# Performance work log

Hardware: AMD Instinct MI355X
Metric: run time of the kernel (lower is better)

## Reference

```python
import jax, jax.numpy as jnp
import numpy as np

DIM = 768
HEADS = 12
DHEAD = 64
N = 197  # 1 cls token + 14*14 patches
P = 196
KMAX = 9  # max neighborhood size (interior patch: 3x3 window)
SCALE = DHEAD ** -0.5


def _build_neighbors():
    """Reproduce the module's hard-coded kv_list; pad to KMAX with a mask."""
    top = set(range(2, 14))
    down = set(range(184, 196))
    left = set(range(15, 170, 14))
    right = set(range(28, 183, 14))
    idx = np.zeros((P, KMAX), np.int32)
    msk = np.zeros((P, KMAX), np.float32)
    for i in range(1, 197):
        if i == 1:
            nb = [1, 2, 15, 16]
        elif i == 14:
            nb = [13, 14, 27, 28]
        elif i == 183:
            nb = [169, 170, 183, 184]
        elif i == 196:
            nb = [181, 182, 195, 196]
        elif i in top:
            nb = [i - 1, i, i + 1, i + 13, i + 14, i + 15]
        elif i in left:
            nb = [i - 14, i - 13, i, i + 1, i + 14, i + 15]
        elif i in right:
            nb = [i - 15, i - 14, i - 1, i, i + 13, i + 14]
        elif i in down:
            nb = [i - 15, i - 14, i - 13, i - 1, i, i + 1]
        else:
            nb = [i - 15, i - 14, i - 13, i - 1, i, i + 1, i + 13, i + 14, i + 15]
        L = len(nb)
        idx[i - 1, :L] = nb
        msk[i - 1, :L] = 1.0
    return jnp.asarray(idx), jnp.asarray(msk)

NBR_IDX, NBR_MASK = _build_neighbors()


def setup_inputs() -> dict:
    key = jax.random.key(0)
    ks = jax.random.split(key, 10)
    b = 128
    w = lambda k: jax.random.normal(k, (DIM, DIM), jnp.float32) * 0.02
    bia = lambda k: jax.random.normal(k, (DIM,), jnp.float32) * 0.02
    return {
        "x_qkv": jax.random.normal(ks[0], (b, N, DIM), jnp.float32),
        "y_q": jax.random.normal(ks[1], (b, N, DIM), jnp.float32),
        "Wq": w(ks[2]), "bq": bia(ks[3]),
        "Wk": w(ks[4]), "bk": bia(ks[5]),
        "Wv": w(ks[6]), "bv": bia(ks[7]),
        "Wo": w(ks[8]), "bo": bia(ks[9]),
    }


def reference(x_qkv, y_q, Wq, bq, Wk, bk, Wv, bv, Wo, bo):
    b = x_qkv.shape[0]
    split = lambda t: t.reshape(b, N, HEADS, DHEAD).transpose(0, 2, 1, 3)  # b h n d
    k = split(x_qkv @ Wk + bk)
    v = split(x_qkv @ Wv + bv)
    q = split(y_q @ Wq + bq)

    # token 0 (cls): full attention over all N keys
    dots0 = jnp.einsum('bhd,bhjd->bhj', q[:, :, 0], k) * SCALE
    out0 = jnp.einsum('bhj,bhjd->bhd', jax.nn.softmax(dots0, axis=-1), v)[:, :, None]  # b h 1 d

    # patches 1..196: gather local windows (padded to KMAX, masked)
    kn = k[:, :, NBR_IDX]  # b h P KMAX d
    vn = v[:, :, NBR_IDX]
    dots = jnp.einsum('bhpd,bhpjd->bhpj', q[:, :, 1:], kn) * SCALE
    big_neg = jnp.asarray(jnp.finfo(dots.dtype).min, dots.dtype)
    dots = jnp.where(NBR_MASK > 0, dots, big_neg)
    attn = jax.nn.softmax(dots, axis=-1)
    outp = jnp.einsum('bhpj,bhpjd->bhpd', attn, vn)  # b h P d

    out = jnp.concatenate([out0, outp], axis=2)           # b h N d
    out = out.transpose(0, 2, 1, 3).reshape(b, N, HEADS * DHEAD)
    return out @ Wo + bo  # dropout: eval mode (identity)
```

## Files before the change

### kernel.cpp

```cpp
#include <hip/hip_runtime.h>


typedef __bf16 bf16x8 __attribute__((ext_vector_type(8)));
typedef float f32x4 __attribute__((ext_vector_type(4)));

#define NTOK 197
#define BATCH 128
#define MROWS (BATCH * NTOK)
#define MTILES_FULL (MROWS / 128)
#define NB_FULL (6 * MTILES_FULL)
#define W_ELEMS ((size_t)768 * 768)
#define BUF_ELEMS_FULL ((size_t)MROWS * 768)
#define PATCH_NBLK (BATCH * 49 * 12 / 4)

#define CHUNK_B 8
#define NCHUNK 16
#define MC_CHUNK (CHUNK_B * NTOK)
#define MTILES_CHUNK 13
#define BUF_ELEMS_CHUNK ((size_t)MC_CHUNK * 768)

__device__ __forceinline__ unsigned short f2b(float f) {
  unsigned int x = __float_as_uint(f);
  x += 0x7fff + ((x >> 16) & 1);
  return (unsigned short)(x >> 16);
}

__device__ __forceinline__ uint4 cvt8pack(float4 f0, float4 f1) {
  unsigned short t8[8] = { f2b(f0.x), f2b(f0.y), f2b(f0.z), f2b(f0.w),
                           f2b(f1.x), f2b(f1.y), f2b(f1.z), f2b(f1.w) };
  return *(const uint4*)t8;
}

#define GLOAD_LDS16(gp, lp)                                                   \
  __builtin_amdgcn_global_load_lds(                                           \
      (const __attribute__((address_space(1))) void*)(gp),                    \
      (__attribute__((address_space(3))) void*)(lp), 16, 0, 0)

__device__ __forceinline__ int xcd_swizzle(int bid, int nb) {
  const int q = nb >> 3, r = nb & 7;
  const int xcd = bid & 7, i = bid >> 3;
  return (xcd < r ? xcd * (q + 1) : r * (q + 1) + (xcd - r) * q) + i;
}

__global__ void transpose768x4(const float* __restrict__ s0, const float* __restrict__ s1,
                               const float* __restrict__ s2, const float* __restrict__ s3,
                               unsigned short* __restrict__ d0, unsigned short* __restrict__ d1,
                               unsigned short* __restrict__ d2, unsigned short* __restrict__ d3) {
  const float* src;
  unsigned short* dst;
  switch (blockIdx.y) {
    case 0: src = s0; dst = d0; break;
    case 1: src = s1; dst = d1; break;
    case 2: src = s2; dst = d2; break;
    default: src = s3; dst = d3; break;
  }
  int idx = blockIdx.x * 256 + threadIdx.x;
  int n = idx / 768, k = idx % 768;
  dst[idx] = f2b(src[k * 768 + n]);
}

__global__ void cvt8(const float* __restrict__ src, unsigned short* __restrict__ dst,
                     const int n8) {
  int i = blockIdx.x * 256 + threadIdx.x;
  if (i >= n8) return;
  const float4* p = (const float4*)(src + (size_t)i * 8);
  *(uint4*)(dst + (size_t)i * 8) = cvt8pack(p[0], p[1]);
}

__device__ __forceinline__ void mfma_tile(const unsigned short* sA, const unsigned short* sB,
                                          f32x4 (&acc)[4][4],
                                          const int wr, const int wc,
                                          const int lane16, const int quad) {
  bf16x8 af[4], bf_[4];
  #pragma unroll
  for (int i = 0; i < 4; ++i)
    af[i] = *(const bf16x8*)&sA[(wr * 64 + i * 16 + lane16) * 32 + quad * 8];
  #pragma unroll
  for (int j = 0; j < 4; ++j)
    bf_[j] = *(const bf16x8*)&sB[(wc * 64 + j * 16 + lane16) * 32 + quad * 8];
  #pragma unroll
  for (int i = 0; i < 4; ++i)
    #pragma unroll
    for (int j = 0; j < 4; ++j)
      acc[i][j] = __builtin_amdgcn_mfma_f32_16x16x32_bf16(af[i], bf_[j], acc[i][j], 0, 0, 0);
}

__device__ __forceinline__ void epilogue128(f32x4 (&acc)[4][4], const float* __restrict__ bias,
                                            float* __restrict__ C, const int row0, const int n0,
                                            const int wr, const int wc,
                                            const int lane16, const int quad) {
  #pragma unroll
  for (int j = 0; j < 4; ++j) {
    const int col = n0 + wc * 64 + j * 16 + lane16;
    const float bv = bias[col];
    #pragma unroll
    for (int i = 0; i < 4; ++i) {
      const int r0 = row0 + wr * 64 + i * 16 + quad * 4;
      #pragma unroll
      for (int r = 0; r < 4; ++r)
        C[(size_t)(r0 + r) * 768 + col] = acc[i][j][r] + bv;
    }
  }
}

__global__ __launch_bounds__(256, 4) void gemm_bf16(
    const unsigned short* __restrict__ A, const unsigned short* __restrict__ Bt,
    const float* __restrict__ bias, float* __restrict__ C) {
  __shared__ unsigned short lds[2][2][4096];
  const int swz = xcd_swizzle(blockIdx.x, NB_FULL);
  const int by = swz / 6, bx = swz % 6;
  const int row0 = by * 128, n0 = bx * 128;
  const int tid = threadIdx.x;
  const int l = tid & 63, w = tid >> 6;
  const int wr = w >> 1, wc = w & 1;
  const int lane16 = l & 15, quad = l >> 4;
  const int rr = tid >> 2, c8 = (tid & 3) * 8;
  const int wbase = (tid & 192) * 8;

  const unsigned short* a0 = A + (size_t)(row0 + rr) * 768 + c8;
  const unsigned short* a1 = a0 + (size_t)64 * 768;
  const unsigned short* b0 = Bt + (size_t)(n0 + rr) * 768 + c8;
  const unsigned short* b1 = b0 + (size_t)64 * 768;

  f32x4 acc[4][4] = {};

#define STAGE_G(B, kt) do { const int ko = (kt) * 32;             \
    GLOAD_LDS16(a0 + ko, &lds[B][0][wbase]);                      \
    GLOAD_LDS16(a1 + ko, &lds[B][0][wbase + 2048]);               \
    GLOAD_LDS16(b0 + ko, &lds[B][1][wbase]);                      \
    GLOAD_LDS16(b1 + ko, &lds[B][1][wbase + 2048]); } while (0)

  STAGE_G(0, 0);
  int cur = 0;
  for (int kt = 0; kt < 23; ++kt) {
    STAGE_G(cur ^ 1, kt + 1);
    asm volatile("s_waitcnt vmcnt(4)" ::: "memory");
    __builtin_amdgcn_s_barrier();
    __builtin_amdgcn_sched_barrier(0);
    mfma_tile(&lds[cur][0][0], &lds[cur][1][0], acc, wr, wc, lane16, quad);
    __builtin_amdgcn_s_barrier();
    cur ^= 1;
  }
  asm volatile("s_waitcnt vmcnt(0)" ::: "memory");
  __builtin_amdgcn_s_barrier();
  __builtin_amdgcn_sched_barrier(0);
  mfma_tile(&lds[cur][0][0], &lds[cur][1][0], acc, wr, wc, lane16, quad);
#undef STAGE_G

  epilogue128(acc, bias, C, row0, n0, wr, wc, lane16, quad);
}

__device__ __forceinline__ void gemm_body_f32A(
    const float* __restrict__ A, const unsigned short* __restrict__ Wt,
    const float* __restrict__ bias, float* __restrict__ C,
    const int row0, const int n0, const int Mrows, unsigned short* sAB) {
  const int tid = threadIdx.x;
  const int l = tid & 63, w = tid >> 6;
  const int wr = w >> 1, wc = w & 1;
  const int lane16 = l & 15, quad = l >> 4;

  f32x4 acc[4][4] = {};

  for (int kt = 0; kt < 24; ++kt) {
    const int k0 = kt * 32;
    #pragma unroll
    for (int i = 0; i < 2; ++i) {
      const int ch = i * 256 + tid;
      const int rr2 = ch >> 2;
      const int c82 = (ch & 3) * 8;
      int ra = row0 + rr2; if (ra > Mrows - 1) ra = Mrows - 1;
      const float* ap = A + (size_t)ra * 768 + k0 + c82;
      float4 q0 = *(const float4*)ap;
      float4 q1 = *(const float4*)(ap + 4);
      *(uint4*)&sAB[rr2 * 32 + c82] = cvt8pack(q0, q1);
      uint4 vb = *(const uint4*)(Wt + (size_t)(n0 + rr2) * 768 + k0 + c82);
      *(uint4*)&sAB[4096 + rr2 * 32 + c82] = vb;
    }
    __syncthreads();
    mfma_tile(sAB, sAB + 4096, acc, wr, wc, lane16, quad);
    __syncthreads();
  }
  #pragma unroll
  for (int j = 0; j < 4; ++j) {
    const int col = n0 + wc * 64 + j * 16 + lane16;
    const float bv = bias[col];
    #pragma unroll
    for (int i = 0; i < 4; ++i) {
      const int r0 = row0 + wr * 64 + i * 16 + quad * 4;
      #pragma unroll
      for (int r = 0; r < 4; ++r)
        if (r0 + r < Mrows)
          C[(size_t)(r0 + r) * 768 + col] = acc[i][j][r] + bv;
    }
  }
}

__global__ __launch_bounds__(256, 2) void qkv_gemm(
    const float* __restrict__ X, const float* __restrict__ Y,
    const unsigned short* __restrict__ WkT, const unsigned short* __restrict__ WvT,
    const unsigned short* __restrict__ WqT,
    const float* __restrict__ bk, const float* __restrict__ bv, const float* __restrict__ bq,
    float* __restrict__ K, float* __restrict__ V, float* __restrict__ Q,
    const int Mrows) {
  __shared__ unsigned short sAB[8192];
  const int mat = blockIdx.x / 6;
  const int n0 = (blockIdx.x % 6) * 128;
  const float* A = (mat == 2) ? Y : X;
  const unsigned short* Wt = (mat == 0) ? WkT : (mat == 1) ? WvT : WqT;
  const float* bias = (mat == 0) ? bk : (mat == 1) ? bv : bq;
  float* C = (mat == 0) ? K : (mat == 1) ? V : Q;
  gemm_body_f32A(A, Wt, bias, C, blockIdx.y * 128, n0, Mrows, sAB);
}

__global__ __launch_bounds__(256, 2) void gemm_bt(
    const float* __restrict__ A, const unsigned short* __restrict__ Wt,
    const float* __restrict__ bias, float* __restrict__ C, const int Mrows) {
  __shared__ unsigned short sAB[8192];
  gemm_body_f32A(A, Wt, bias, C, blockIdx.y * 128, blockIdx.x * 128, Mrows, sAB);
}

__global__ void cls_attn_b(const float* __restrict__ Q, const float* __restrict__ K,
                           const float* __restrict__ V, unsigned short* __restrict__ ATT) {
  __shared__ float q[64];
  __shared__ float attn[256];
  __shared__ float red[8];
  __shared__ float part[4][64];
  const int tid = threadIdx.x, l = tid & 63, w = tid >> 6;
  const int b = blockIdx.x / 12, h = blockIdx.x % 12;
  const size_t rowbase = ((size_t)b * NTOK) * 768 + h * 64;

  if (tid < 64) q[tid] = Q[rowbase + tid];
  __syncthreads();

  float d = -3e38f;
  if (tid < NTOK) {
    const float4* Kp = (const float4*)(K + rowbase + (size_t)tid * 768);
    float s = 0.f;
    #pragma unroll
    for (int u = 0; u < 16; ++u) {
      float4 kk = Kp[u];
      s += q[u * 4 + 0] * kk.x + q[u * 4 + 1] * kk.y
         + q[u * 4 + 2] * kk.z + q[u * 4 + 3] * kk.w;
    }
    d = s * 0.125f;
  }
  float m = d;
  #pragma unroll
  for (int off = 32; off; off >>= 1) m = fmaxf(m, __shfl_xor(m, off, 64));
  if (l == 0) red[w] = m;
  __syncthreads();
  const float M = fmaxf(fmaxf(red[0], red[1]), fmaxf(red[2], red[3]));
  float e = (tid < NTOK) ? __expf(d - M) : 0.f;
  float ssum = e;
  #pragma unroll
  for (int off = 32; off; off >>= 1) ssum += __shfl_xor(ssum, off, 64);
  if (l == 0) red[4 + w] = ssum;
  __syncthreads();
  const float S = red[4] + red[5] + red[6] + red[7];
  attn[tid] = e / S;
  __syncthreads();

  const int dd = tid & 63, jg = tid >> 6;
  float o = 0.f;
  for (int j = jg; j < NTOK; j += 4)
    o += attn[j] * V[rowbase + (size_t)j * 768 + dd];
  part[jg][dd] = o;
  __syncthreads();
  if (tid < 64) {
    const float r = part[0][tid] + part[1][tid] + part[2][tid] + part[3][tid];
    ATT[rowbase + tid] = f2b(r);
  }
}

__device__ __forceinline__ float cls_attn_body(const float* __restrict__ Q,
                                               const float* __restrict__ K,
                                               const float* __restrict__ V,
                                               const size_t rowbase,
                                               float* q, float* attn, float* red) {
  const int tid = threadIdx.x, l = tid & 63, w = tid >> 6;
  if (tid < 64) q[tid] = Q[rowbase + tid];
  __syncthreads();

  float d = -3e38f;
  if (tid < NTOK) {
    const float4* Kp = (const float4*)(K + rowbase + (size_t)tid * 768);
    float s = 0.f;
    #pragma unroll
    for (int u = 0; u < 16; ++u) {
      float4 kk = Kp[u];
      s += q[u * 4 + 0] * kk.x + q[u * 4 + 1] * kk.y
         + q[u * 4 + 2] * kk.z + q[u * 4 + 3] * kk.w;
    }
    d = s * 0.125f;
  }
  float m = d;
  #pragma unroll
  for (int off = 32; off; off >>= 1) m = fmaxf(m, __shfl_xor(m, off, 64));
  if (l == 0) red[w] = m;
  __syncthreads();
  const float M = fmaxf(fmaxf(red[0], red[1]), fmaxf(red[2], red[3]));
  float e = (tid < NTOK) ? __expf(d - M) : 0.f;
  float ssum = e;
  #pragma unroll
  for (int off = 32; off; off >>= 1) ssum += __shfl_xor(ssum, off, 64);
  if (l == 0) red[4 + w] = ssum;
  __syncthreads();
  const float S = red[4] + red[5] + red[6] + red[7];
  attn[tid] = e / S;
  __syncthreads();
  float o = 0.f;
  if (tid < 64) {
    for (int j = 0; j < NTOK; ++j)
      o += attn[j] * V[rowbase + (size_t)j * 768 + tid];
  }
  return o;
}

__global__ void cls_attn(const float* __restrict__ Q, const float* __restrict__ K,
                         const float* __restrict__ V, float* __restrict__ ATT) {
  __shared__ float q[64];
  __shared__ float attn[256];
  __shared__ float red[8];
  const int b = blockIdx.x / 12, h = blockIdx.x % 12;
  const size_t rowbase = ((size_t)b * NTOK) * 768 + h * 64;
  float o = cls_attn_body(Q, K, V, rowbase, q, attn, red);
  if (threadIdx.x < 64) ATT[rowbase + threadIdx.x] = o;
}

__global__ __launch_bounds__(256) void patch_attn4_b(
    const float* __restrict__ Q, const float* __restrict__ K,
    const float* __restrict__ V, unsigned short* __restrict__ ATT) {
  const int swb = xcd_swizzle(blockIdx.x, PATCH_NBLK);
  const int wu = swb * 4 + (threadIdx.x >> 6);
  const int l = threadIdx.x & 63;
  const int t16 = l & 15, pg = l >> 4;
  const int h = wu % 12;
  const int t2 = wu / 12;
  const int pq = t2 % 49;
  const int b = t2 / 49;
  const int p = pq * 4 + pg;
  const int r = p / 14, c = p % 14;
  const size_t ib = ((size_t)b * NTOK) * 768 + h * 64 + t16 * 4;

  const float4 q = *(const float4*)(Q + ib + (size_t)(p + 1) * 768);

  float s[9];
  int tok[9];
  #pragma unroll
  for (int jj = 0; jj < 9; ++jj) {
    const int nr = r + jj / 3 - 1, nc = c + jj % 3 - 1;
    const bool ok = ((unsigned)nr < 14u) && ((unsigned)nc < 14u);
    tok[jj] = ok ? (1 + nr * 14 + nc) : (p + 1);
    const float4 kk = *(const float4*)(K + ib + (size_t)tok[jj] * 768);
    float d = q.x * kk.x + q.y * kk.y + q.z * kk.z + q.w * kk.w;
    d += __shfl_xor(d, 1);
    d += __shfl_xor(d, 2);
    d += __shfl_xor(d, 4);
    d += __shfl_xor(d, 8);
    s[jj] = ok ? d * 0.125f : -3e38f;
  }
  float m = s[0];
  #pragma unroll
  for (int jj = 1; jj < 9; ++jj) m = fmaxf(m, s[jj]);
  float sum = 0.f;
  #pragma unroll
  for (int jj = 0; jj < 9; ++jj) { s[jj] = __expf(s[jj] - m); sum += s[jj]; }
  const float inv = 1.f / sum;

  float4 o = {0.f, 0.f, 0.f, 0.f};
  #pragma unroll
  for (int jj = 0; jj < 9; ++jj) {
    const float4 vv = *(const float4*)(V + ib + (size_t)tok[jj] * 768);
    o.x += s[jj] * vv.x; o.y += s[jj] * vv.y;
    o.z += s[jj] * vv.z; o.w += s[jj] * vv.w;
  }
  o.x *= inv; o.y *= inv; o.z *= inv; o.w *= inv;
  unsigned short t4[4] = { f2b(o.x), f2b(o.y), f2b(o.z), f2b(o.w) };
  *(ushort2*)&ATT[ib + (size_t)(p + 1) * 768] = *(const ushort2*)&t4[0];
  *(ushort2*)&ATT[ib + (size_t)(p + 1) * 768 + 2] = *(const ushort2*)&t4[2];
}

__device__ __forceinline__ float patch_attn_body(const float* __restrict__ Q,
                                                 const float* __restrict__ K,
                                                 const float* __restrict__ V,
                                                 const size_t base, const int p,
                                                 const int r, const int c) {
  const float qd = Q[base + (size_t)(p + 1) * 768];

  float s[9];
  int tok[9];
  #pragma unroll
  for (int jj = 0; jj < 9; ++jj) {
    const int nr = r + jj / 3 - 1, nc = c + jj % 3 - 1;
    const bool ok = ((unsigned)nr < 14u) && ((unsigned)nc < 14u);
    tok[jj] = ok ? (1 + nr * 14 + nc) : (p + 1);
    float d = qd * K[base + (size_t)tok[jj] * 768];
    #pragma unroll
    for (int off = 32; off; off >>= 1) d += __shfl_xor(d, off, 64);
    s[jj] = ok ? d * 0.125f : -3e38f;
  }
  float m = s[0];
  #pragma unroll
  for (int jj = 1; jj < 9; ++jj) m = fmaxf(m, s[jj]);
  float sum = 0.f;
  #pragma unroll
  for (int jj = 0; jj < 9; ++jj) { s[jj] = __expf(s[jj] - m); sum += s[jj]; }
  const float inv = 1.f / sum;
  float o = 0.f;
  #pragma unroll
  for (int jj = 0; jj < 9; ++jj) o += s[jj] * V[base + (size_t)tok[jj] * 768];
  return o * inv;
}

__global__ void patch_attn(const float* __restrict__ Q, const float* __restrict__ K,
                           const float* __restrict__ V, float* __restrict__ ATT) {
  const int wgid = blockIdx.x * 4 + (threadIdx.x >> 6);
  const int l = threadIdx.x & 63;
  const int h = wgid % 12;
  const int t2 = wgid / 12;
  const int p = t2 % 196;
  const int b = t2 / 196;
  const int r = p / 14, c = p % 14;
  const size_t base = ((size_t)b * NTOK) * 768 + h * 64 + l;
  float o = patch_attn_body(Q, K, V, base, p, r, c);
  ATT[base + (size_t)(p + 1) * 768] = o;
}

extern "C" void kernel_launch(void* const* d_in, const int* in_sizes, int n_in,
                              void* d_out, int out_size, void* d_ws, size_t ws_size,
                              hipStream_t stream) {
  const float* x  = (const float*)d_in[0];
  const float* y  = (const float*)d_in[1];
  const float* Wq = (const float*)d_in[2];
  const float* bq = (const float*)d_in[3];
  const float* Wk = (const float*)d_in[4];
  const float* bk = (const float*)d_in[5];
  const float* Wv = (const float*)d_in[6];
  const float* bv = (const float*)d_in[7];
  const float* Wo = (const float*)d_in[8];
  const float* bo = (const float*)d_in[9];
  float* out = (float*)d_out;

  unsigned short* WqT = (unsigned short*)d_ws;
  unsigned short* WkT = WqT + W_ELEMS;
  unsigned short* WvT = WkT + W_ELEMS;
  unsigned short* WoT = WvT + W_ELEMS;

  transpose768x4<<<dim3(2304, 4), 256, 0, stream>>>(Wq, Wk, Wv, Wo, WqT, WkT, WvT, WoT);

  const size_t need_full = 4 * W_ELEMS * sizeof(unsigned short)
                         + BUF_ELEMS_FULL * sizeof(unsigned short)
                         + 3 * BUF_ELEMS_FULL * sizeof(float);
  if (ws_size >= need_full) {
    unsigned short* R1 = WoT + W_ELEMS;
    float* Kc = (float*)(R1 + BUF_ELEMS_FULL);
    float* Vc = Kc + BUF_ELEMS_FULL;
    float* Qc = Vc + BUF_ELEMS_FULL;

    const int n8 = (int)(BUF_ELEMS_FULL / 8);
    cvt8<<<n8 / 256, 256, 0, stream>>>(x, R1, n8);
    gemm_bf16<<<NB_FULL, 256, 0, stream>>>(R1, WkT, bk, Kc);
    gemm_bf16<<<NB_FULL, 256, 0, stream>>>(R1, WvT, bv, Vc);
    cvt8<<<n8 / 256, 256, 0, stream>>>(y, R1, n8);
    gemm_bf16<<<NB_FULL, 256, 0, stream>>>(R1, WqT, bq, Qc);
    cls_attn_b<<<BATCH * 12, 256, 0, stream>>>(Qc, Kc, Vc, R1);
    patch_attn4_b<<<PATCH_NBLK, 256, 0, stream>>>(Qc, Kc, Vc, R1);
    gemm_bf16<<<NB_FULL, 256, 0, stream>>>(R1, WoT, bo, out);
  } else {
    float* Kc = (float*)(WoT + W_ELEMS);
    float* Vc = Kc + BUF_ELEMS_CHUNK;
    float* Qc = Vc + BUF_ELEMS_CHUNK;

    for (int c = 0; c < NCHUNK; ++c) {
      const float* xc = x + (size_t)c * BUF_ELEMS_CHUNK;
      const float* yc = y + (size_t)c * BUF_ELEMS_CHUNK;
      qkv_gemm<<<dim3(18, MTILES_CHUNK), 256, 0, stream>>>(
          xc, yc, WkT, WvT, WqT, bk, bv, bq, Kc, Vc, Qc, MC_CHUNK);
      cls_attn<<<CHUNK_B * 12, 256, 0, stream>>>(Qc, Kc, Vc, Qc);
      patch_attn<<<(CHUNK_B * 196 * 12) / 4, 256, 0, stream>>>(Qc, Kc, Vc, Qc);
      gemm_bt<<<dim3(6, MTILES_CHUNK), 256, 0, stream>>>(Qc, WoT, bo,
                                                         out + (size_t)c * BUF_ELEMS_CHUNK, MC_CHUNK);
    }
  }
}
```

Measured before the change: 511.9 us.

## Triple-buffer GEMM pipeline, merge K/V GEMMs, stage patch-attention windows in LDS

Moves the bf16 GEMM from a two-stage to a three-stage LDS pipeline so global loads run two k-steps ahead, and lowers occupancy to 3 blocks to make room for the extra buffer. The K and V projections now share one launch with twice the blocks, which removes one kernel launch and tail effect. Patch attention now processes a two-row strip of patches per block: it loads the needed K/V rows (including halo rows) into LDS once, so each of the 9 neighbour reads hits LDS instead of global memory. The cost is a larger LDS footprint per block, less occupancy in the GEMM, and a block-wide sync in the attention kernel.

```diff
diff --git a/kernel.cpp b/kernel.cpp
--- a/kernel.cpp
+++ b/kernel.cpp
@@ -9,9 +9,11 @@
 #define MROWS (BATCH * NTOK)
 #define MTILES_FULL (MROWS / 128)
 #define NB_FULL (6 * MTILES_FULL)
+#define NB_KV (2 * NB_FULL)
 #define W_ELEMS ((size_t)768 * 768)
 #define BUF_ELEMS_FULL ((size_t)MROWS * 768)
-#define PATCH_NBLK (BATCH * 49 * 12 / 4)
+#define PSTRIPS 7
+#define PATCH2_NBLK (BATCH * PSTRIPS * 12)
 
 #define CHUNK_B 8
 #define NCHUNK 16
@@ -103,13 +105,10 @@
   }
 }
 
-__global__ __launch_bounds__(256, 4) void gemm_bf16(
+__device__ __forceinline__ void gemm_core3(
     const unsigned short* __restrict__ A, const unsigned short* __restrict__ Bt,
-    const float* __restrict__ bias, float* __restrict__ C) {
-  __shared__ unsigned short lds[2][2][4096];
-  const int swz = xcd_swizzle(blockIdx.x, NB_FULL);
-  const int by = swz / 6, bx = swz % 6;
-  const int row0 = by * 128, n0 = bx * 128;
+    const float* __restrict__ bias, float* __restrict__ C,
+    const int row0, const int n0, unsigned short* lds) {
   const int tid = threadIdx.x;
   const int l = tid & 63, w = tid >> 6;
   const int wr = w >> 1, wc = w & 1;
@@ -124,30 +123,63 @@
 
   f32x4 acc[4][4] = {};
 
-#define STAGE_G(B, kt) do { const int ko = (kt) * 32;             \
-    GLOAD_LDS16(a0 + ko, &lds[B][0][wbase]);                      \
-    GLOAD_LDS16(a1 + ko, &lds[B][0][wbase + 2048]);               \
-    GLOAD_LDS16(b0 + ko, &lds[B][1][wbase]);                      \
-    GLOAD_LDS16(b1 + ko, &lds[B][1][wbase + 2048]); } while (0)
-
-  STAGE_G(0, 0);
-  int cur = 0;
-  for (int kt = 0; kt < 23; ++kt) {
-    STAGE_G(cur ^ 1, kt + 1);
-    asm volatile("s_waitcnt vmcnt(4)" ::: "memory");
+#define STAGE3(B, kt) do { const int ko = (kt) * 32;                  \
+    unsigned short* lb = lds + (B) * 8192;                            \
+    GLOAD_LDS16(a0 + ko, lb + wbase);                                 \
+    GLOAD_LDS16(a1 + ko, lb + wbase + 2048);                          \
+    GLOAD_LDS16(b0 + ko, lb + 4096 + wbase);                          \
+    GLOAD_LDS16(b1 + ko, lb + 4096 + wbase + 2048); } while (0)
+
+  STAGE3(0, 0);
+  STAGE3(1, 1);
+  int cur = 0, stg = 2;
+  for (int kt = 0; kt < 22; ++kt) {
+    STAGE3(stg, kt + 2);
+    asm volatile("s_waitcnt vmcnt(8)" ::: "memory");
     __builtin_amdgcn_s_barrier();
     __builtin_amdgcn_sched_barrier(0);
-    mfma_tile(&lds[cur][0][0], &lds[cur][1][0], acc, wr, wc, lane16, quad);
+    mfma_tile(lds + cur * 8192, lds + cur * 8192 + 4096, acc, wr, wc, lane16, quad);
     __builtin_amdgcn_s_barrier();
-    cur ^= 1;
-  }
+    cur = (cur == 2) ? 0 : cur + 1;
+    stg = (stg == 2) ? 0 : stg + 1;
+  }
+  asm volatile("s_waitcnt vmcnt(4)" ::: "memory");
+  __builtin_amdgcn_s_barrier();
+  __builtin_amdgcn_sched_barrier(0);
+  mfma_tile(lds + cur * 8192, lds + cur * 8192 + 4096, acc, wr, wc, lane16, quad);
+  cur = (cur == 2) ? 0 : cur + 1;
   asm volatile("s_waitcnt vmcnt(0)" ::: "memory");
   __builtin_amdgcn_s_barrier();
   __builtin_amdgcn_sched_barrier(0);
-  mfma_tile(&lds[cur][0][0], &lds[cur][1][0], acc, wr, wc, lane16, quad);
-#undef STAGE_G
+  mfma_tile(lds + cur * 8192, lds + cur * 8192 + 4096, acc, wr, wc, lane16, quad);
+#undef STAGE3
 
   epilogue128(acc, bias, C, row0, n0, wr, wc, lane16, quad);
+}
+
+__global__ __launch_bounds__(256, 3) void gemm_bf16(
+    const unsigned short* __restrict__ A, const unsigned short* __restrict__ Bt,
+    const float* __restrict__ bias, float* __restrict__ C) {
+  __shared__ unsigned short lds[3 * 8192];
+  const int swz = xcd_swizzle(blockIdx.x, NB_FULL);
+  const int by = swz / 6, bx = swz % 6;
+  gemm_core3(A, Bt, bias, C, by * 128, bx * 128, lds);
+}
+
+__global__ __launch_bounds__(256, 3) void gemm_bf16_kv(
+    const unsigned short* __restrict__ Xb,
+    const unsigned short* __restrict__ WkT, const unsigned short* __restrict__ WvT,
+    const float* __restrict__ bk, const float* __restrict__ bv,
+    float* __restrict__ K, float* __restrict__ V) {
+  __shared__ unsigned short lds[3 * 8192];
+  const int swz = xcd_swizzle(blockIdx.x, NB_KV);
+  const int by = swz / 12;
+  const int rem = swz % 12;
+  const int mat = rem / 6, bx = rem % 6;
+  const unsigned short* Bt = mat ? WvT : WkT;
+  const float* bias = mat ? bv : bk;
+  float* C = mat ? V : K;
+  gemm_core3(Xb, Bt, bias, C, by * 128, bx * 128, lds);
 }
 
 __device__ __forceinline__ void gemm_body_f32A(
@@ -327,57 +359,81 @@
   if (threadIdx.x < 64) ATT[rowbase + threadIdx.x] = o;
 }
 
-__global__ __launch_bounds__(256) void patch_attn4_b(
+__global__ __launch_bounds__(448, 7) void patch_attn_lds(
     const float* __restrict__ Q, const float* __restrict__ K,
     const float* __restrict__ V, unsigned short* __restrict__ ATT) {
-  const int swb = xcd_swizzle(blockIdx.x, PATCH_NBLK);
-  const int wu = swb * 4 + (threadIdx.x >> 6);
-  const int l = threadIdx.x & 63;
+  __shared__ float Kl[4 * 14 * 64];
+  __shared__ float Vl[4 * 14 * 64];
+  const int bid = xcd_swizzle(blockIdx.x, PATCH2_NBLK);
+  const int h = bid % 12;
+  const int t2 = bid / 12;
+  const int s = t2 % PSTRIPS;
+  const int b = t2 / PSTRIPS;
+  const int tid = threadIdx.x;
+
+  {
+    const int fi = tid * 8;
+    const int lr = fi / 896;
+    const int rem = fi - lr * 896;
+    const int tr = s * 2 - 1 + lr;
+    if ((unsigned)tr < 14u) {
+      const int tok = 1 + tr * 14 + (rem >> 6);
+      const unsigned goff = (unsigned)((b * NTOK + tok) * 768 + h * 64 + (rem & 63));
+      *(float4*)&Kl[fi]     = *(const float4*)(K + goff);
+      *(float4*)&Kl[fi + 4] = *(const float4*)(K + goff + 4);
+      *(float4*)&Vl[fi]     = *(const float4*)(V + goff);
+      *(float4*)&Vl[fi + 4] = *(const float4*)(V + goff + 4);
+    }
+  }
+  __syncthreads();
+
+  const int l = tid & 63;
   const int t16 = l & 15, pg = l >> 4;
-  const int h = wu % 12;
-  const int t2 = wu / 12;
-  const int pq = t2 % 49;
-  const int b = t2 / 49;
-  const int p = pq * 4 + pg;
-  const int r = p / 14, c = p % 14;
-  const size_t ib = ((size_t)b * NTOK) * 768 + h * 64 + t16 * 4;
-
-  const float4 q = *(const float4*)(Q + ib + (size_t)(p + 1) * 768);
-
-  float s[9];
-  int tok[9];
+  const int lp = (tid >> 6) * 4 + pg;
+  const int prl = lp / 14, pc = lp - prl * 14;
+  const int r = s * 2 + prl, c = pc;
+  const int p = r * 14 + c;
+  const unsigned qoff = (unsigned)((b * NTOK + p + 1) * 768 + h * 64 + t16 * 4);
+
+  const float4 q = *(const float4*)(Q + qoff);
+
+  float s9[9];
+  int loff[9];
   #pragma unroll
   for (int jj = 0; jj < 9; ++jj) {
-    const int nr = r + jj / 3 - 1, nc = c + jj % 3 - 1;
+    const int dj = jj / 3, dc = jj % 3 - 1;
+    const int nr = r + dj - 1, nc = c + dc;
     const bool ok = ((unsigned)nr < 14u) && ((unsigned)nc < 14u);
-    tok[jj] = ok ? (1 + nr * 14 + nc) : (p + 1);
-    const float4 kk = *(const float4*)(K + ib + (size_t)tok[jj] * 768);
+    const int lr = ok ? (prl + dj) : (prl + 1);
+    const int lc = ok ? nc : c;
+    loff[jj] = (lr * 14 + lc) * 64 + t16 * 4;
+    const float4 kk = *(const float4*)&Kl[loff[jj]];
     float d = q.x * kk.x + q.y * kk.y + q.z * kk.z + q.w * kk.w;
     d += __shfl_xor(d, 1);
     d += __shfl_xor(d, 2);
     d += __shfl_xor(d, 4);
     d += __shfl_xor(d, 8);
-    s[jj] = ok ? d * 0.125f : -3e38f;
-  }
-  float m = s[0];
-  #pragma unroll
-  for (int jj = 1; jj < 9; ++jj) m = fmaxf(m, s[jj]);
+    s9[jj] = ok ? d * 0.125f : -3e38f;
+  }
+  float m = s9[0];
+  #pragma unroll
+  for (int jj = 1; jj < 9; ++jj) m = fmaxf(m, s9[jj]);
   float sum = 0.f;
   #pragma unroll
-  for (int jj = 0; jj < 9; ++jj) { s[jj] = __expf(s[jj] - m); sum += s[jj]; }
+  for (int jj = 0; jj < 9; ++jj) { s9[jj] = __expf(s9[jj] - m); sum += s9[jj]; }
   const float inv = 1.f / sum;
 
   float4 o = {0.f, 0.f, 0.f, 0.f};
   #pragma unroll
   for (int jj = 0; jj < 9; ++jj) {
-    const float4 vv = *(const float4*)(V + ib + (size_t)tok[jj] * 768);
-    o.x += s[jj] * vv.x; o.y += s[jj] * vv.y;
-    o.z += s[jj] * vv.z; o.w += s[jj] * vv.w;
+    const float4 vv = *(const float4*)&Vl[loff[jj]];
+    o.x += s9[jj] * vv.x; o.y += s9[jj] * vv.y;
+    o.z += s9[jj] * vv.z; o.w += s9[jj] * vv.w;
   }
   o.x *= inv; o.y *= inv; o.z *= inv; o.w *= inv;
   unsigned short t4[4] = { f2b(o.x), f2b(o.y), f2b(o.z), f2b(o.w) };
-  *(ushort2*)&ATT[ib + (size_t)(p + 1) * 768] = *(const ushort2*)&t4[0];
-  *(ushort2*)&ATT[ib + (size_t)(p + 1) * 768 + 2] = *(const ushort2*)&t4[2];
+  *(ushort2*)&ATT[qoff] = *(const ushort2*)&t4[0];
+  *(ushort2*)&ATT[qoff + 2] = *(const ushort2*)&t4[2];
 }
 
 __device__ __forceinline__ float patch_attn_body(const float* __restrict__ Q,
@@ -459,12 +515,11 @@
 
     const int n8 = (int)(BUF_ELEMS_FULL / 8);
     cvt8<<<n8 / 256, 256, 0, stream>>>(x, R1, n8);
-    gemm_bf16<<<NB_FULL, 256, 0, stream>>>(R1, WkT, bk, Kc);
-    gemm_bf16<<<NB_FULL, 256, 0, stream>>>(R1, WvT, bv, Vc);
+    gemm_bf16_kv<<<NB_KV, 256, 0, stream>>>(R1, WkT, WvT, bk, bv, Kc, Vc);
     cvt8<<<n8 / 256, 256, 0, stream>>>(y, R1, n8);
     gemm_bf16<<<NB_FULL, 256, 0, stream>>>(R1, WqT, bq, Qc);
     cls_attn_b<<<BATCH * 12, 256, 0, stream>>>(Qc, Kc, Vc, R1);
-    patch_attn4_b<<<PATCH_NBLK, 256, 0, stream>>>(Qc, Kc, Vc, R1);
+    patch_attn_lds<<<PATCH2_NBLK, 448, 0, stream>>>(Qc, Kc, Vc, R1);
     gemm_bf16<<<NB_FULL, 256, 0, stream>>>(R1, WoT, bo, out);
   } else {
     float* Kc = (float*)(WoT + W_ELEMS);
```

After: 496.5 us. 1.03x faster.
